# Kernel optimization log

Hardware: AMD Instinct MI355X
Metric: run time of the kernel (lower is better)

The kernel has to match this reference:

```python
import jax, jax.numpy as jnp
import numpy as np

N_NODES = 100000
N_EDGES = 1600000
IN_FEATS = 128
N_HIDDEN = 128
N_CLASSES = 16


def setup_inputs() -> dict:
    key = jax.random.key(0)
    ks = jax.random.split(key, 10)
    features = jax.random.normal(ks[0], (N_NODES, IN_FEATS), dtype=jnp.float32)
    src = jax.random.randint(ks[1], (N_EDGES,), 0, N_NODES, dtype=jnp.int32)
    dst = jax.random.randint(ks[2], (N_EDGES,), 0, N_NODES, dtype=jnp.int32)
    # Glorot-ish init for the three GraphConv layers
    def glorot(k, fan_in, fan_out):
        s = (2.0 / (fan_in + fan_out)) ** 0.5
        return jax.random.normal(k, (fan_in, fan_out), dtype=jnp.float32) * s
    W0 = glorot(ks[3], IN_FEATS, N_HIDDEN)
    b0 = jnp.zeros((N_HIDDEN,), jnp.float32)
    W1 = glorot(ks[4], N_HIDDEN, N_HIDDEN)
    b1 = jnp.zeros((N_HIDDEN,), jnp.float32)
    W2 = glorot(ks[5], N_HIDDEN, N_CLASSES)
    b2 = jnp.zeros((N_CLASSES,), jnp.float32)
    return {"features": features, "src": src, "dst": dst,
            "W0": W0, "b0": b0, "W1": W1, "b1": b1, "W2": W2, "b2": b2}


def _graph_conv(h, src, dst, src_norm, dst_norm, W, b, act):
    # DGL GraphConv, norm='both':
    # out = D_dst^{-1/2} * sum_{(u->v) in E} (D_src^{-1/2} h)_u W  + b
    h = h * src_norm[:, None]           # [N, F] scale by out-degree^-1/2
    hw = h @ W                          # [N, F_out] transform before gather (F_out <= F here)
    agg = jax.ops.segment_sum(hw[src], dst, num_segments=h.shape[0])  # scatter-add over edges
    out = agg * dst_norm[:, None] + b
    return act(out)


def reference(features, src, dst, W0, b0, W1, b1, W2, b2):
    N = features.shape[0]
    ones = jnp.ones(src.shape[0], dtype=jnp.float32)
    out_deg = jnp.clip(jax.ops.segment_sum(ones, src, num_segments=N), 1.0)
    in_deg = jnp.clip(jax.ops.segment_sum(ones, dst, num_segments=N), 1.0)
    src_norm = out_deg ** -0.5
    dst_norm = in_deg ** -0.5

    relu = jax.nn.relu
    pos_sigmoid = lambda x: jax.nn.sigmoid(x) + 1e-8

    h = features.astype(jnp.float32)
    h = _graph_conv(h, src, dst, src_norm, dst_norm, W0, b0, relu)
    h = _graph_conv(h, src, dst, src_norm, dst_norm, W1, b1, relu)
    h = _graph_conv(h, src, dst, src_norm, dst_norm, W2, b2, pos_sigmoid)
    return h
```

## Files before the change

### kernel.cpp

```cpp
#include <hip/hip_runtime.h>
#include <hip/hip_bf16.h>


constexpr int BLK = 256;
constexpr int CH = 8192;

typedef __attribute__((ext_vector_type(8))) short s8v;
typedef __attribute__((ext_vector_type(4))) float f4v;

__device__ __forceinline__ float bflo(unsigned int u) { return __uint_as_float(u << 16); }
__device__ __forceinline__ float bfhi(unsigned int u) { return __uint_as_float(u & 0xffff0000u); }
__device__ __forceinline__ unsigned int bfr(float f) {
    unsigned int u = __float_as_uint(f);
    return (u + 0x7fffu + ((u >> 16) & 1u)) >> 16;
}
__device__ __forceinline__ unsigned int bfpack(float lo, float hi) {
    unsigned int ul = __float_as_uint(lo), uh = __float_as_uint(hi);
    unsigned int rl = (ul + 0x7fffu + ((ul >> 16) & 1u)) >> 16;
    unsigned int rh = (uh + 0x7fffu + ((uh >> 16) & 1u)) & 0xffff0000u;
    return rl | rh;
}

__global__ __launch_bounds__(256) void k_pcount(const int* __restrict__ src, const int* __restrict__ dst,
                                                int* __restrict__ pmat_d, int* __restrict__ pmat_s,
                                                int E, int NB) {
    __shared__ int hd[1024], hs[1024];
    for (int i = threadIdx.x; i < 1024; i += 256) { hd[i] = 0; hs[i] = 0; }
    __syncthreads();
    int b = blockIdx.x;
    int e0 = b * CH, e1 = min(e0 + CH, E);
    for (int e = e0 + threadIdx.x; e < e1; e += 256) {
        atomicAdd(&hd[dst[e] >> 7], 1);
        atomicAdd(&hs[src[e] >> 7], 1);
    }
    __syncthreads();
    for (int i = threadIdx.x; i < NB; i += 256) {
        pmat_d[(size_t)b * NB + i] = hd[i];
        pmat_s[(size_t)b * NB + i] = hs[i];
    }
}

__global__ __launch_bounds__(1024) void k_pscan(const int* __restrict__ pmat_d, const int* __restrict__ pmat_s,
                                                int* __restrict__ bbase_d, int* __restrict__ bbase_s,
                                                int* __restrict__ omat_d, int* __restrict__ omat_s,
                                                unsigned short* __restrict__ B2pad, unsigned short* __restrict__ HW16pad,
                                                int N, int NB, int nblk) {
    const int* pmat = blockIdx.x ? pmat_s : pmat_d;
    int* bbase = blockIdx.x ? bbase_s : bbase_d;
    int* omat  = blockIdx.x ? omat_s : omat_d;
    __shared__ int s[1024];
    int t = threadIdx.x;
    int tot = 0;
    if (t < NB) {
#pragma unroll 8
        for (int b = 0; b < nblk; b++) tot += pmat[(size_t)b * NB + t];
    }
    s[t] = (t < NB) ? tot : 0;
    __syncthreads();
    for (int d = 1; d < 1024; d <<= 1) {
        int x = (t >= d) ? s[t - d] : 0;
        __syncthreads();
        s[t] += x;
        __syncthreads();
    }
    if (t < NB) {
        int base = s[t] - tot;
        bbase[t] = base;
        if (t == NB - 1) bbase[NB] = s[t];
        int run = base;
#pragma unroll 8
        for (int b = 0; b < nblk; b++) {
            size_t idx = (size_t)b * NB + t;
            omat[idx] = run;
            run += pmat[idx];
        }
    }
    if (blockIdx.x == 1) {
        if (t < 128) B2pad[(size_t)N * 128 + t] = 0;
        if (t < 16)  HW16pad[(size_t)N * 16 + t] = 0;
    }
}

__global__ __launch_bounds__(256) void k_pscatter(const int* __restrict__ src, const int* __restrict__ dst,
                                                  const int* __restrict__ omat_d, const int* __restrict__ omat_s,
                                                  unsigned int* __restrict__ ebuf_d, unsigned char* __restrict__ ebuf_s,
                                                  int E, int NB) {
    __shared__ int cd[1024], cs[1024];
    int b = blockIdx.x;
    for (int i = threadIdx.x; i < NB; i += 256) {
        cd[i] = omat_d[(size_t)b * NB + i];
        cs[i] = omat_s[(size_t)b * NB + i];
    }
    __syncthreads();
    int e0 = b * CH, e1 = min(e0 + CH, E);
    for (int e = e0 + threadIdx.x; e < e1; e += 256) {
        int s_ = src[e], d_ = dst[e];
        int pd = atomicAdd(&cd[d_ >> 7], 1);
        ebuf_d[pd] = (unsigned)s_ | ((unsigned)(d_ & 127) << 17);
        int ps = atomicAdd(&cs[s_ >> 7], 1);
        ebuf_s[ps] = (unsigned char)(s_ & 127);
    }
}

__global__ __launch_bounds__(256) void k_build(const unsigned int* __restrict__ ebuf_d,
                                               const int* __restrict__ bbase_d,
                                               const unsigned char* __restrict__ ebuf_s,
                                               const int* __restrict__ bbase_s,
                                               int* __restrict__ csr, int* __restrict__ rowptr,
                                               int* __restrict__ deg, float* __restrict__ srcn,
                                               const float* __restrict__ W0, const float* __restrict__ W1,
                                               const float* __restrict__ W2,
                                               unsigned short* __restrict__ Wt0, unsigned short* __restrict__ Wt1,
                                               unsigned short* __restrict__ Wt2,
                                               int N, int NB) {
    int b = blockIdx.x, tx = threadIdx.x;
    if (b < NB) {
        __shared__ unsigned int rec[3584];
        __shared__ unsigned int sorted[4096];
        __shared__ int cnt[128];
        __shared__ int pws[129];
        __shared__ int wcur[128];
        int k = b;
        int ebeg = bbase_d[k];
        int ecnt = bbase_d[k + 1] - ebeg;
        if (ecnt > 3584) ecnt = 3584;
        int pbase = ((ebeg + 3) & ~3) + k * 512;
        if (tx < 128) cnt[tx] = 0;
        __syncthreads();
        for (int i = tx; i < ecnt; i += 256) {
            unsigned int r = ebuf_d[ebeg + i];
            rec[i] = r;
            atomicAdd(&cnt[(r >> 17) & 127], 1);
        }
        __syncthreads();
        int pc = (tx < 128) ? ((cnt[tx] + 3) & ~3) : 0;
        if (tx < 128) wcur[tx] = pc;
        __syncthreads();
        for (int d = 1; d < 128; d <<= 1) {
            int x = (tx < 128 && tx >= d) ? wcur[tx - d] : 0;
            __syncthreads();
            if (tx < 128) wcur[tx] += x;
            __syncthreads();
        }
        if (tx < 128) pws[tx] = wcur[tx] - pc;
        if (tx == 127) pws[128] = wcur[127];
        __syncthreads();
        int pecnt = pws[128];
        for (int i = tx; i < pecnt; i += 256) sorted[i] = (unsigned)N;
        if (tx < 128) wcur[tx] = pws[tx];
        __syncthreads();
        for (int i = tx; i < ecnt; i += 256) {
            unsigned int r = rec[i];
            int p = atomicAdd(&wcur[(r >> 17) & 127], 1);
            sorted[p] = r & 0x1FFFFu;
        }
        __syncthreads();
        for (int i = tx; i < pecnt; i += 256) csr[pbase + i] = (int)sorted[i];
        if (tx < 128) {
            int v = k * 128 + tx;
            if (v < N) { rowptr[v] = pbase + pws[tx]; deg[v] = cnt[tx]; }
        }
    } else if (b < 2 * NB) {
        __shared__ int scnt[128];
        int k = b - NB;
        if (tx < 128) scnt[tx] = 0;
        __syncthreads();
        int beg = bbase_s[k], end = bbase_s[k + 1];
        for (int i = beg + tx; i < end; i += 256) atomicAdd(&scnt[ebuf_s[i]], 1);
        __syncthreads();
        if (tx < 128) {
            int v = k * 128 + tx;
            if (v < N) {
                int c = scnt[tx];
                if (c < 1) c = 1;
                srcn[v] = rsqrtf((float)c);
            }
        }
    } else {
        int bb = b - 2 * NB;
        const float* W; unsigned short* Wt; int total, base;
        if (bb < 64)      { W = W0; Wt = Wt0; total = 16384; base = bb * 256; }
        else if (bb < 128){ W = W1; Wt = Wt1; total = 16384; base = (bb - 64) * 256; }
        else              { W = W2; Wt = Wt2; total = 2048;  base = (bb - 128) * 256; }
        int i = base + tx;
        if (i < total) {
            int Ncol = total >> 7;
            int c = i >> 7, kk = i & 127;
            Wt[i] = (unsigned short)bfr(W[kk * Ncol + c]);
        }
    }
}

template <int NT, int F32IN>
__global__ __launch_bounds__(256) void k_gemm_mfma(const unsigned short* __restrict__ Ab,
                                                   const float* __restrict__ Af,
                                                   const float* __restrict__ srcn,
                                                   const unsigned short* __restrict__ Wt,
                                                   unsigned short* __restrict__ outb, int M) {
    __shared__ unsigned short Ws[NT * 16 * 128];
    __shared__ unsigned short As[64 * 128];
    int tx = threadIdx.x;
    for (int p = 0; p < NT; ++p) {
        int r = p * 16 + (tx >> 4);
        int c = tx & 15;
        int cs = c ^ (r & 7);
        *(uint4*)(&Ws[(r * 16 + cs) * 8]) = *(const uint4*)(Wt + (size_t)r * 128 + c * 8);
    }
    int w = tx >> 6, l = tx & 63;
    int lr = l & 15, lg = l >> 4;
    int ar = w * 16 + lr;

    for (int strip = 0; strip < 4; ++strip) {
        int row0 = blockIdx.x * 256 + strip * 64;
        __syncthreads();
        for (int p = 0; p < 4; ++p) {
            int r = p * 16 + (tx >> 4);
            int c = tx & 15;
            int cs = c ^ (r & 7);
            int gr = row0 + r;
            uint4 v = make_uint4(0u, 0u, 0u, 0u);
            if (gr < M) {
                if (F32IN) {
                    const float4* pf = (const float4*)(Af + (size_t)gr * 128 + c * 8);
                    float4 a = pf[0], bq = pf[1];
                    float s = srcn[gr];
                    v.x = bfpack(a.x * s, a.y * s);
                    v.y = bfpack(a.z * s, a.w * s);
                    v.z = bfpack(bq.x * s, bq.y * s);
                    v.w = bfpack(bq.z * s, bq.w * s);
                } else {
                    v = *(const uint4*)(Ab + (size_t)gr * 128 + c * 8);
                }
            }
            *(uint4*)(&As[(r * 16 + cs) * 8]) = v;
        }
        __syncthreads();

        f4v acc[NT];
#pragma unroll
        for (int nt = 0; nt < NT; ++nt) { acc[nt][0] = 0.f; acc[nt][1] = 0.f; acc[nt][2] = 0.f; acc[nt][3] = 0.f; }
#pragma unroll
        for (int kk = 0; kk < 4; ++kk) {
            s8v af = *(const s8v*)(&As[(ar * 16 + ((kk * 4 + lg) ^ (ar & 7))) * 8]);
#pragma unroll
            for (int nt = 0; nt < NT; ++nt) {
                int br = nt * 16 + lr;
                s8v bf = *(const s8v*)(&Ws[(br * 16 + ((kk * 4 + lg) ^ (br & 7))) * 8]);
                acc[nt] = __builtin_amdgcn_mfma_f32_16x16x32_bf16(af, bf, acc[nt], 0, 0, 0);
            }
        }
#pragma unroll
        for (int nt = 0; nt < NT; ++nt) {
#pragma unroll
            for (int i = 0; i < 4; ++i) {
                int R = row0 + w * 16 + lg * 4 + i;
                if (R < M) {
                    int col = nt * 16 + lr;
                    outb[(size_t)R * (NT * 16) + col] = (unsigned short)bfr(acc[nt][i]);
                }
            }
        }
    }
}

__global__ __launch_bounds__(256) void k_aggN(const unsigned short* __restrict__ hw,
                                              const int* __restrict__ csr,
                                              const int* __restrict__ rowptr,
                                              const int* __restrict__ deg,
                                              const float* __restrict__ srcn,
                                              const float* __restrict__ bias,
                                              unsigned short* __restrict__ out, int N) {
    int t = blockIdx.x * 256 + threadIdx.x;
    int v = t >> 4, sub = t & 15;
    if (v >= N) return;
    int s0 = rowptr[v];
    int dg = deg[v];
    int plen = (dg + 3) & ~3;
    const unsigned short* hws = hw + sub * 8;

    float a0 = 0.f, a1 = 0.f, a2 = 0.f, a3 = 0.f, a4 = 0.f, a5 = 0.f, a6 = 0.f, a7 = 0.f;
#define ACC8(V)                                                         \
    a0 += bflo(V.x); a1 += bfhi(V.x); a2 += bflo(V.y); a3 += bfhi(V.y); \
    a4 += bflo(V.z); a5 += bfhi(V.z); a6 += bflo(V.w); a7 += bfhi(V.w);
    for (int e = s0; e < s0 + plen; e += 4) {
        int4 xs = *(const int4*)(csr + e);
        uint4 v0 = *(const uint4*)(hws + (size_t)xs.x * 128);
        uint4 v1 = *(const uint4*)(hws + (size_t)xs.y * 128);
        uint4 v2 = *(const uint4*)(hws + (size_t)xs.z * 128);
        uint4 v3 = *(const uint4*)(hws + (size_t)xs.w * 128);
        ACC8(v0) ACC8(v1) ACC8(v2) ACC8(v3)
    }
#undef ACC8
    int d = dg < 1 ? 1 : dg;
    float dn = rsqrtf((float)d);
    float4 b0 = *(const float4*)(bias + sub * 8);
    float4 b1 = *(const float4*)(bias + sub * 8 + 4);
    float sn = srcn[v];
    float o0 = fmaxf(a0 * dn + b0.x, 0.f) * sn, o1 = fmaxf(a1 * dn + b0.y, 0.f) * sn;
    float o2 = fmaxf(a2 * dn + b0.z, 0.f) * sn, o3 = fmaxf(a3 * dn + b0.w, 0.f) * sn;
    float o4 = fmaxf(a4 * dn + b1.x, 0.f) * sn, o5 = fmaxf(a5 * dn + b1.y, 0.f) * sn;
    float o6 = fmaxf(a6 * dn + b1.z, 0.f) * sn, o7 = fmaxf(a7 * dn + b1.w, 0.f) * sn;
    uint4 o;
    o.x = bfpack(o0, o1); o.y = bfpack(o2, o3);
    o.z = bfpack(o4, o5); o.w = bfpack(o6, o7);
    *(uint4*)(out + (size_t)v * 128 + sub * 8) = o;
}

__global__ __launch_bounds__(256) void k_agg16(const unsigned short* __restrict__ hw,
                                               const int* __restrict__ csr,
                                               const int* __restrict__ rowptr,
                                               const int* __restrict__ deg,
                                               const float* __restrict__ bias,
                                               float* __restrict__ out, int N) {
    int t = blockIdx.x * 256 + threadIdx.x;
    int v = t >> 2, q = t & 3;
    if (v >= N) return;
    int s0 = rowptr[v];
    int dg = deg[v];
    int plen = (dg + 3) & ~3;
    const unsigned short* hws = hw + q * 4;
    float a0 = 0.f, a1 = 0.f, a2 = 0.f, a3 = 0.f;
#define ACC4(V)                                                         \
    a0 += bflo(V.x); a1 += bfhi(V.x); a2 += bflo(V.y); a3 += bfhi(V.y);
    for (int e = s0; e < s0 + plen; e += 4) {
        int4 xs = *(const int4*)(csr + e);
        uint2 v0 = *(const uint2*)(hws + (size_t)xs.x * 16);
        uint2 v1 = *(const uint2*)(hws + (size_t)xs.y * 16);
        uint2 v2 = *(const uint2*)(hws + (size_t)xs.z * 16);
        uint2 v3 = *(const uint2*)(hws + (size_t)xs.w * 16);
        ACC4(v0) ACC4(v1) ACC4(v2) ACC4(v3)
    }
#undef ACC4
    int d = dg < 1 ? 1 : dg;
    float dn = rsqrtf((float)d);
    float4 b = *(const float4*)(bias + q * 4);
    float o0 = 1.f / (1.f + __expf(-(a0 * dn + b.x))) + 1e-8f;
    float o1 = 1.f / (1.f + __expf(-(a1 * dn + b.y))) + 1e-8f;
    float o2 = 1.f / (1.f + __expf(-(a2 * dn + b.z))) + 1e-8f;
    float o3 = 1.f / (1.f + __expf(-(a3 * dn + b.w))) + 1e-8f;
    *(float4*)(out + (size_t)v * 16 + q * 4) = make_float4(o0, o1, o2, o3);
}

extern "C" void kernel_launch(void* const* d_in, const int* in_sizes, int n_in,
                              void* d_out, int out_size, void* d_ws, size_t ws_size,
                              hipStream_t stream) {
    const float* features = (const float*)d_in[0];
    const int*   src      = (const int*)d_in[1];
    const int*   dst      = (const int*)d_in[2];
    const float* W0       = (const float*)d_in[3];
    const float* b0       = (const float*)d_in[4];
    const float* W1       = (const float*)d_in[5];
    const float* b1       = (const float*)d_in[6];
    const float* W2       = (const float*)d_in[7];
    const float* b2       = (const float*)d_in[8];
    float* out = (float*)d_out;

    const int N = in_sizes[0] / 128;
    const int E = in_sizes[1];
    const int NB = (N + 127) >> 7;
    const int nblk = (E + CH - 1) / CH;

    char* ws = (char*)d_ws;
    size_t off = 0;
    auto alloc = [&](size_t bytes) -> char* {
        char* p = ws + off;
        off += (bytes + 255) / 256 * 256;
        return p;
    };
    int* pmat_d  = (int*)alloc((size_t)nblk * NB * 4);
    int* pmat_s  = (int*)alloc((size_t)nblk * NB * 4);
    int* omat_d  = (int*)alloc((size_t)nblk * NB * 4);
    int* omat_s  = (int*)alloc((size_t)nblk * NB * 4);
    int* bbase_d = (int*)alloc((size_t)(NB + 1) * 4);
    int* bbase_s = (int*)alloc((size_t)(NB + 1) * 4);
    unsigned int*  ebuf_d = (unsigned int*)alloc((size_t)E * 4);
    unsigned char* ebuf_s = (unsigned char*)alloc((size_t)E);
    int* csr     = (int*)alloc(((size_t)E + (size_t)NB * 512 + 512) * 4);
    int* rowptr  = (int*)alloc((size_t)(N + 1) * 4);
    int* deg     = (int*)alloc((size_t)N * 4);
    float* srcn  = (float*)alloc((size_t)N * 4);
    unsigned short* Wt0 = (unsigned short*)alloc(128 * 128 * 2);
    unsigned short* Wt1 = (unsigned short*)alloc(128 * 128 * 2);
    unsigned short* Wt2 = (unsigned short*)alloc(16 * 128 * 2);
    unsigned short* B1 = (unsigned short*)alloc((size_t)N * 128 * 2);
    unsigned short* B2 = (unsigned short*)alloc((size_t)(N + 1) * 128 * 2);
    unsigned short* HW16 = (unsigned short*)alloc((size_t)(N + 1) * 16 * 2);
    (void)ws_size; (void)n_in; (void)out_size;

    k_pcount<<<nblk, 256, 0, stream>>>(src, dst, pmat_d, pmat_s, E, NB);
    k_pscan<<<2, 1024, 0, stream>>>(pmat_d, pmat_s, bbase_d, bbase_s, omat_d, omat_s, B2, HW16, N, NB, nblk);
    k_pscatter<<<nblk, 256, 0, stream>>>(src, dst, omat_d, omat_s, ebuf_d, ebuf_s, E, NB);
    k_build<<<2 * NB + 136, 256, 0, stream>>>(ebuf_d, bbase_d, ebuf_s, bbase_s, csr, rowptr, deg, srcn,
                                              W0, W1, W2, Wt0, Wt1, Wt2, N, NB);

    int gb = (N + 255) / 256;
    int anb = (N * 16 + 255) / 256;
    int a16b = (N * 4 + 255) / 256;

    k_gemm_mfma<8, 1><<<gb, 256, 0, stream>>>(nullptr, features, srcn, Wt0, B2, N);
    k_aggN<<<anb, 256, 0, stream>>>(B2, csr, rowptr, deg, srcn, b0, B1, N);
    k_gemm_mfma<8, 0><<<gb, 256, 0, stream>>>(B1, nullptr, nullptr, Wt1, B2, N);
    k_aggN<<<anb, 256, 0, stream>>>(B2, csr, rowptr, deg, srcn, b1, B1, N);
    k_gemm_mfma<1, 0><<<gb, 256, 0, stream>>>(B1, nullptr, nullptr, Wt2, HW16, N);
    k_agg16<<<a16b, 256, 0, stream>>>(HW16, csr, rowptr, deg, b2, out, N);
}
```

Measured before the change: 357.8 us.

## Store hidden features as 16-column slabs to localize gathers in aggregation

```diff
diff --git a/kernel.cpp b/kernel.cpp
--- a/kernel.cpp
+++ b/kernel.cpp
@@ -76,7 +76,7 @@
         }
     }
     if (blockIdx.x == 1) {
-        if (t < 128) B2pad[(size_t)N * 128 + t] = 0;
+        if (t < 128) B2pad[((size_t)(t >> 4) * (N + 1) + N) * 16 + (t & 15)] = 0;
         if (t < 16)  HW16pad[(size_t)N * 16 + t] = 0;
     }
 }
@@ -213,14 +213,14 @@
     for (int strip = 0; strip < 4; ++strip) {
         int row0 = blockIdx.x * 256 + strip * 64;
         __syncthreads();
-        for (int p = 0; p < 4; ++p) {
-            int r = p * 16 + (tx >> 4);
-            int c = tx & 15;
-            int cs = c ^ (r & 7);
-            int gr = row0 + r;
-            uint4 v = make_uint4(0u, 0u, 0u, 0u);
-            if (gr < M) {
-                if (F32IN) {
+        if (F32IN) {
+            for (int p = 0; p < 4; ++p) {
+                int r = p * 16 + (tx >> 4);
+                int c = tx & 15;
+                int cs = c ^ (r & 7);
+                int gr = row0 + r;
+                uint4 v = make_uint4(0u, 0u, 0u, 0u);
+                if (gr < M) {
                     const float4* pf = (const float4*)(Af + (size_t)gr * 128 + c * 8);
                     float4 a = pf[0], bq = pf[1];
                     float s = srcn[gr];
@@ -228,11 +228,21 @@
                     v.y = bfpack(a.z * s, a.w * s);
                     v.z = bfpack(bq.x * s, bq.y * s);
                     v.w = bfpack(bq.z * s, bq.w * s);
-                } else {
-                    v = *(const uint4*)(Ab + (size_t)gr * 128 + c * 8);
                 }
+                *(uint4*)(&As[(r * 16 + cs) * 8]) = v;
             }
-            *(uint4*)(&As[(r * 16 + cs) * 8]) = v;
+        } else {
+            for (int lq = 0; lq < 4; ++lq) {
+                int f = tx + lq * 256;
+                int pl = f >> 7;
+                int j = f & 127;
+                int r = j >> 1, hf = j & 1;
+                int gr = row0 + r;
+                uint4 v = make_uint4(0u, 0u, 0u, 0u);
+                if (gr < M) v = *(const uint4*)(Ab + ((size_t)pl * (M + 1) + gr) * 16 + hf * 8);
+                int c = pl * 2 + hf;
+                *(uint4*)(&As[(r * 16 + (c ^ (r & 7))) * 8]) = v;
+            }
         }
         __syncthreads();
 
@@ -255,28 +265,29 @@
             for (int i = 0; i < 4; ++i) {
                 int R = row0 + w * 16 + lg * 4 + i;
                 if (R < M) {
-                    int col = nt * 16 + lr;
-                    outb[(size_t)R * (NT * 16) + col] = (unsigned short)bfr(acc[nt][i]);
+                    outb[((size_t)nt * (M + 1) + R) * 16 + lr] = (unsigned short)bfr(acc[nt][i]);
                 }
             }
         }
     }
 }
 
-__global__ __launch_bounds__(256) void k_aggN(const unsigned short* __restrict__ hw,
+__global__ __launch_bounds__(256) void k_aggS(const unsigned short* __restrict__ hw,
                                               const int* __restrict__ csr,
                                               const int* __restrict__ rowptr,
                                               const int* __restrict__ deg,
                                               const float* __restrict__ srcn,
                                               const float* __restrict__ bias,
                                               unsigned short* __restrict__ out, int N) {
-    int t = blockIdx.x * 256 + threadIdx.x;
-    int v = t >> 4, sub = t & 15;
+    int s = blockIdx.x & 7;
+    int r = blockIdx.x >> 3;
+    int idx = r * 256 + threadIdx.x;
+    int v = idx >> 1, half = idx & 1;
     if (v >= N) return;
     int s0 = rowptr[v];
     int dg = deg[v];
     int plen = (dg + 3) & ~3;
-    const unsigned short* hws = hw + sub * 8;
+    const unsigned short* hws = hw + (size_t)s * (N + 1) * 16 + half * 8;
 
     float a0 = 0.f, a1 = 0.f, a2 = 0.f, a3 = 0.f, a4 = 0.f, a5 = 0.f, a6 = 0.f, a7 = 0.f;
 #define ACC8(V)                                                         \
@@ -284,17 +295,18 @@
     a4 += bflo(V.z); a5 += bfhi(V.z); a6 += bflo(V.w); a7 += bfhi(V.w);
     for (int e = s0; e < s0 + plen; e += 4) {
         int4 xs = *(const int4*)(csr + e);
-        uint4 v0 = *(const uint4*)(hws + (size_t)xs.x * 128);
-        uint4 v1 = *(const uint4*)(hws + (size_t)xs.y * 128);
-        uint4 v2 = *(const uint4*)(hws + (size_t)xs.z * 128);
-        uint4 v3 = *(const uint4*)(hws + (size_t)xs.w * 128);
+        uint4 v0 = *(const uint4*)(hws + (size_t)xs.x * 16);
+        uint4 v1 = *(const uint4*)(hws + (size_t)xs.y * 16);
+        uint4 v2 = *(const uint4*)(hws + (size_t)xs.z * 16);
+        uint4 v3 = *(const uint4*)(hws + (size_t)xs.w * 16);
         ACC8(v0) ACC8(v1) ACC8(v2) ACC8(v3)
     }
 #undef ACC8
     int d = dg < 1 ? 1 : dg;
     float dn = rsqrtf((float)d);
-    float4 b0 = *(const float4*)(bias + sub * 8);
-    float4 b1 = *(const float4*)(bias + sub * 8 + 4);
+    int col = s * 16 + half * 8;
+    float4 b0 = *(const float4*)(bias + col);
+    float4 b1 = *(const float4*)(bias + col + 4);
     float sn = srcn[v];
     float o0 = fmaxf(a0 * dn + b0.x, 0.f) * sn, o1 = fmaxf(a1 * dn + b0.y, 0.f) * sn;
     float o2 = fmaxf(a2 * dn + b0.z, 0.f) * sn, o3 = fmaxf(a3 * dn + b0.w, 0.f) * sn;
@@ -303,7 +315,7 @@
     uint4 o;
     o.x = bfpack(o0, o1); o.y = bfpack(o2, o3);
     o.z = bfpack(o4, o5); o.w = bfpack(o6, o7);
-    *(uint4*)(out + (size_t)v * 128 + sub * 8) = o;
+    *(uint4*)(out + ((size_t)s * (N + 1) + v) * 16 + half * 8) = o;
 }
 
 __global__ __launch_bounds__(256) void k_agg16(const unsigned short* __restrict__ hw,
@@ -382,7 +394,7 @@
     unsigned short* Wt0 = (unsigned short*)alloc(128 * 128 * 2);
     unsigned short* Wt1 = (unsigned short*)alloc(128 * 128 * 2);
     unsigned short* Wt2 = (unsigned short*)alloc(16 * 128 * 2);
-    unsigned short* B1 = (unsigned short*)alloc((size_t)N * 128 * 2);
+    unsigned short* B1 = (unsigned short*)alloc((size_t)(N + 1) * 128 * 2);
     unsigned short* B2 = (unsigned short*)alloc((size_t)(N + 1) * 128 * 2);
     unsigned short* HW16 = (unsigned short*)alloc((size_t)(N + 1) * 16 * 2);
     (void)ws_size; (void)n_in; (void)out_size;
@@ -394,13 +406,14 @@
                                               W0, W1, W2, Wt0, Wt1, Wt2, N, NB);
 
     int gb = (N + 255) / 256;
-    int anb = (N * 16 + 255) / 256;
+    int bps = (2 * N + 255) / 256;
+    int asb = bps * 8;
     int a16b = (N * 4 + 255) / 256;
 
     k_gemm_mfma<8, 1><<<gb, 256, 0, stream>>>(nullptr, features, srcn, Wt0, B2, N);
-    k_aggN<<<anb, 256, 0, stream>>>(B2, csr, rowptr, deg, srcn, b0, B1, N);
+    k_aggS<<<asb, 256, 0, stream>>>(B2, csr, rowptr, deg, srcn, b0, B1, N);
     k_gemm_mfma<8, 0><<<gb, 256, 0, stream>>>(B1, nullptr, nullptr, Wt1, B2, N);
-    k_aggN<<<anb, 256, 0, stream>>>(B2, csr, rowptr, deg, srcn, b1, B1, N);
+    k_aggS<<<asb, 256, 0, stream>>>(B2, csr, rowptr, deg, srcn, b1, B1, N);
     k_gemm_mfma<1, 0><<<gb, 256, 0, stream>>>(B1, nullptr, nullptr, Wt2, HW16, N);
     k_agg16<<<a16b, 256, 0, stream>>>(HW16, csr, rowptr, deg, b2, out, N);
 }
```

New measurement: 415.2 us. 1.16x slower.

## Register-resident GEMM with double-buffered A loads and unroll aggregation by 8

Applied to the files above, without the earlier changes.

```diff
diff --git a/kernel.cpp b/kernel.cpp
--- a/kernel.cpp
+++ b/kernel.cpp
@@ -192,75 +192,85 @@
 }
 
 template <int NT, int F32IN>
-__global__ __launch_bounds__(256) void k_gemm_mfma(const unsigned short* __restrict__ Ab,
-                                                   const float* __restrict__ Af,
-                                                   const float* __restrict__ srcn,
-                                                   const unsigned short* __restrict__ Wt,
-                                                   unsigned short* __restrict__ outb, int M) {
-    __shared__ unsigned short Ws[NT * 16 * 128];
-    __shared__ unsigned short As[64 * 128];
+__global__ __launch_bounds__(256, 2) void k_gemm_mfma(const unsigned short* __restrict__ Ab,
+                                                      const float* __restrict__ Af,
+                                                      const float* __restrict__ srcn,
+                                                      const unsigned short* __restrict__ Wt,
+                                                      unsigned short* __restrict__ outb, int M) {
     int tx = threadIdx.x;
-    for (int p = 0; p < NT; ++p) {
-        int r = p * 16 + (tx >> 4);
-        int c = tx & 15;
-        int cs = c ^ (r & 7);
-        *(uint4*)(&Ws[(r * 16 + cs) * 8]) = *(const uint4*)(Wt + (size_t)r * 128 + c * 8);
-    }
     int w = tx >> 6, l = tx & 63;
     int lr = l & 15, lg = l >> 4;
-    int ar = w * 16 + lr;
-
-    for (int strip = 0; strip < 4; ++strip) {
-        int row0 = blockIdx.x * 256 + strip * 64;
-        __syncthreads();
-        for (int p = 0; p < 4; ++p) {
-            int r = p * 16 + (tx >> 4);
-            int c = tx & 15;
-            int cs = c ^ (r & 7);
-            int gr = row0 + r;
-            uint4 v = make_uint4(0u, 0u, 0u, 0u);
-            if (gr < M) {
-                if (F32IN) {
-                    const float4* pf = (const float4*)(Af + (size_t)gr * 128 + c * 8);
-                    float4 a = pf[0], bq = pf[1];
-                    float s = srcn[gr];
-                    v.x = bfpack(a.x * s, a.y * s);
-                    v.y = bfpack(a.z * s, a.w * s);
-                    v.z = bfpack(bq.x * s, bq.y * s);
-                    v.w = bfpack(bq.z * s, bq.w * s);
-                } else {
-                    v = *(const uint4*)(Ab + (size_t)gr * 128 + c * 8);
-                }
-            }
-            *(uint4*)(&As[(r * 16 + cs) * 8]) = v;
-        }
-        __syncthreads();
-
-        f4v acc[NT];
+    int wbase = (blockIdx.x * 4 + w) * 64;
+
+    s8v bf[NT][4];
 #pragma unroll
-        for (int nt = 0; nt < NT; ++nt) { acc[nt][0] = 0.f; acc[nt][1] = 0.f; acc[nt][2] = 0.f; acc[nt][3] = 0.f; }
+    for (int nt = 0; nt < NT; ++nt) {
+        int br = nt * 16 + lr;
 #pragma unroll
-        for (int kk = 0; kk < 4; ++kk) {
-            s8v af = *(const s8v*)(&As[(ar * 16 + ((kk * 4 + lg) ^ (ar & 7))) * 8]);
-#pragma unroll
-            for (int nt = 0; nt < NT; ++nt) {
-                int br = nt * 16 + lr;
-                s8v bf = *(const s8v*)(&Ws[(br * 16 + ((kk * 4 + lg) ^ (br & 7))) * 8]);
-                acc[nt] = __builtin_amdgcn_mfma_f32_16x16x32_bf16(af, bf, acc[nt], 0, 0, 0);
-            }
-        }
-#pragma unroll
-        for (int nt = 0; nt < NT; ++nt) {
-#pragma unroll
-            for (int i = 0; i < 4; ++i) {
-                int R = row0 + w * 16 + lg * 4 + i;
-                if (R < M) {
-                    int col = nt * 16 + lr;
-                    outb[(size_t)R * (NT * 16) + col] = (unsigned short)bfr(acc[nt][i]);
-                }
-            }
-        }
-    }
+        for (int kk = 0; kk < 4; ++kk)
+            bf[nt][kk] = *(const s8v*)(Wt + (size_t)br * 128 + (kk * 4 + lg) * 8);
+    }
+
+    union U { uint4 u; s8v v; };
+    U bufA[4], bufB[4];
+
+#define LOADA(S, DST)                                                          \
+    {                                                                          \
+        int r0_ = wbase + (S) * 16 + lr;                                       \
+        if (r0_ < M) {                                                         \
+            if (F32IN) {                                                       \
+                float sn_ = srcn[r0_];                                         \
+                _Pragma("unroll")                                              \
+                for (int kk = 0; kk < 4; ++kk) {                               \
+                    const float4* pf = (const float4*)(Af + (size_t)r0_ * 128 + (kk * 4 + lg) * 8); \
+                    float4 x = pf[0], y = pf[1];                               \
+                    DST[kk].u.x = bfpack(x.x * sn_, x.y * sn_);                \
+                    DST[kk].u.y = bfpack(x.z * sn_, x.w * sn_);                \
+                    DST[kk].u.z = bfpack(y.x * sn_, y.y * sn_);                \
+                    DST[kk].u.w = bfpack(y.z * sn_, y.w * sn_);                \
+                }                                                              \
+            } else {                                                           \
+                _Pragma("unroll")                                              \
+                for (int kk = 0; kk < 4; ++kk)                                 \
+                    DST[kk].u = *(const uint4*)(Ab + (size_t)r0_ * 128 + (kk * 4 + lg) * 8); \
+            }                                                                  \
+        } else {                                                               \
+            _Pragma("unroll")                                                  \
+            for (int kk = 0; kk < 4; ++kk) DST[kk].u = make_uint4(0u, 0u, 0u, 0u); \
+        }                                                                      \
+    }
+
+#define COMPUTE(S, CUR)                                                        \
+    {                                                                          \
+        f4v acc[NT];                                                           \
+        _Pragma("unroll")                                                      \
+        for (int nt = 0; nt < NT; ++nt) { acc[nt][0] = 0.f; acc[nt][1] = 0.f; acc[nt][2] = 0.f; acc[nt][3] = 0.f; } \
+        _Pragma("unroll")                                                      \
+        for (int kk = 0; kk < 4; ++kk) {                                       \
+            _Pragma("unroll")                                                  \
+            for (int nt = 0; nt < NT; ++nt)                                    \
+                acc[nt] = __builtin_amdgcn_mfma_f32_16x16x32_bf16(CUR[kk].v, bf[nt][kk], acc[nt], 0, 0, 0); \
+        }                                                                      \
+        _Pragma("unroll")                                                      \
+        for (int nt = 0; nt < NT; ++nt) {                                      \
+            _Pragma("unroll")                                                  \
+            for (int i = 0; i < 4; ++i) {                                      \
+                int R = wbase + (S) * 16 + lg * 4 + i;                         \
+                if (R < M) outb[(size_t)R * (NT * 16) + nt * 16 + lr] = (unsigned short)bfr(acc[nt][i]); \
+            }                                                                  \
+        }                                                                      \
+    }
+
+    LOADA(0, bufA)
+    LOADA(1, bufB)
+    COMPUTE(0, bufA)
+    LOADA(2, bufA)
+    COMPUTE(1, bufB)
+    LOADA(3, bufB)
+    COMPUTE(2, bufA)
+    COMPUTE(3, bufB)
+#undef LOADA
+#undef COMPUTE
 }
 
 __global__ __launch_bounds__(256) void k_aggN(const unsigned short* __restrict__ hw,
@@ -282,7 +292,22 @@
 #define ACC8(V)                                                         \
     a0 += bflo(V.x); a1 += bfhi(V.x); a2 += bflo(V.y); a3 += bfhi(V.y); \
     a4 += bflo(V.z); a5 += bfhi(V.z); a6 += bflo(V.w); a7 += bfhi(V.w);
-    for (int e = s0; e < s0 + plen; e += 4) {
+    int e = s0;
+    int end8 = s0 + (plen & ~7);
+    for (; e < end8; e += 8) {
+        int4 xa = *(const int4*)(csr + e);
+        int4 xb = *(const int4*)(csr + e + 4);
+        uint4 v0 = *(const uint4*)(hws + (size_t)xa.x * 128);
+        uint4 v1 = *(const uint4*)(hws + (size_t)xa.y * 128);
+        uint4 v2 = *(const uint4*)(hws + (size_t)xa.z * 128);
+        uint4 v3 = *(const uint4*)(hws + (size_t)xa.w * 128);
+        uint4 v4 = *(const uint4*)(hws + (size_t)xb.x * 128);
+        uint4 v5 = *(const uint4*)(hws + (size_t)xb.y * 128);
+        uint4 v6 = *(const uint4*)(hws + (size_t)xb.z * 128);
+        uint4 v7 = *(const uint4*)(hws + (size_t)xb.w * 128);
+        ACC8(v0) ACC8(v1) ACC8(v2) ACC8(v3) ACC8(v4) ACC8(v5) ACC8(v6) ACC8(v7)
+    }
+    if (plen & 4) {
         int4 xs = *(const int4*)(csr + e);
         uint4 v0 = *(const uint4*)(hws + (size_t)xs.x * 128);
         uint4 v1 = *(const uint4*)(hws + (size_t)xs.y * 128);
```

After: 357.5 us. No clear change (-0.1%).
